# Optimization experiments

Measured on AMD Instinct MI355X. Metric: run time of the kernel, lower is better.

The kernel has to match this reference:

```python
import jax, jax.numpy as jnp
import numpy as np

DIM = 2048
N_HEADS = 16
HEAD_DIM = DIM // N_HEADS
# torch.nn.RMSNorm(eps=None) uses torch.finfo(fp32).eps
RMS_EPS = 1.1920928955078125e-07


def rmsnorm(x, weight):
    # x: [..., Hd]; normalize over last dim, learned scale
    var = jnp.mean(jnp.square(x), axis=-1, keepdims=True)
    return x * jax.lax.rsqrt(var + RMS_EPS) * weight


def setup_inputs() -> dict:
    key = jax.random.key(0)
    ks = jax.random.split(key, 10)
    B, T, D = 4, 2048, DIM
    s = 1.0 / np.sqrt(D)
    return {
        "x": jax.random.normal(ks[0], (B, T, D), dtype=jnp.float32),
        "Wq": jax.random.normal(ks[1], (D, D), dtype=jnp.float32) * s,
        "bq": jnp.zeros((D,), dtype=jnp.float32),
        "Wk": jax.random.normal(ks[2], (D, D), dtype=jnp.float32) * s,
        "bk": jnp.zeros((D,), dtype=jnp.float32),
        "Wv": jax.random.normal(ks[3], (D, D), dtype=jnp.float32) * s,
        "bv": jnp.zeros((D,), dtype=jnp.float32),
        "q_norm_w": jnp.ones((HEAD_DIM,), dtype=jnp.float32),
        "k_norm_w": jnp.ones((HEAD_DIM,), dtype=jnp.float32),
        "Wo": jax.random.normal(ks[4], (D, D), dtype=jnp.float32) * s,
        "bo": jnp.zeros((D,), dtype=jnp.float32),
    }


def reference(x, Wq, bq, Wk, bk, Wv, bv, q_norm_w, k_norm_w, Wo, bo):
    B, T, D = x.shape
    H, Hd = N_HEADS, HEAD_DIM
    # Q/K/V projections (torch Linear: x @ W.T + b)
    q = (x @ Wq.T + bq).reshape(B, T, H, Hd)
    k = (x @ Wk.T + bk).reshape(B, T, H, Hd)
    v = (x @ Wv.T + bv).reshape(B, T, H, Hd)
    # per-head RMSNorm on Q and K
    q = rmsnorm(q, q_norm_w)
    k = rmsnorm(k, k_norm_w)
    # full (non-causal) attention per batch element; scale = 1/sqrt(Hd)
    scale = 1.0 / np.sqrt(Hd)
    scores = jnp.einsum("bqhd,bkhd->bhqk", q, k) * scale
    probs = jax.nn.softmax(scores, axis=-1)
    out = jnp.einsum("bhqk,bkhd->bqhd", probs, v).reshape(B, T, D)
    return out @ Wo.T + bo
```

## Files before the change

### kernel.cpp

```cpp
#include <hip/hip_runtime.h>
#include <cstddef>
#include <cstdint>


typedef __attribute__((ext_vector_type(8))) short sh8;
typedef __attribute__((ext_vector_type(4))) float fx4;
typedef __attribute__((ext_vector_type(4))) unsigned short us4;
typedef __attribute__((ext_vector_type(4))) float f4;
typedef __attribute__((ext_vector_type(2))) unsigned uix2;
typedef unsigned short u16;

#define DEVI __device__ __forceinline__

DEVI u16 f2bf(float f) {
  union { float f; unsigned u; } v; v.f = f;
  return (u16)((v.u + 0x7FFFu + ((v.u >> 16) & 1u)) >> 16);
}
DEVI float bf2f(u16 h) {
  union { unsigned u; float f; } v; v.u = ((unsigned)h) << 16;
  return v.f;
}
DEVI void gload16(const void* g, void* l) {
  __builtin_amdgcn_global_load_lds((const __attribute__((address_space(1))) void*)g,
                                   (__attribute__((address_space(3))) void*)l, 16, 0, 0);
}

__global__ __launch_bounds__(256) void k_cvt(const float* __restrict__ in,
                                             u16* __restrict__ out, int n4) {
  int i = blockIdx.x * 256 + threadIdx.x;
  if (i >= n4) return;
  f4 v = ((const f4*)in)[i];
  us4 o;
  o[0] = f2bf(v[0]); o[1] = f2bf(v[1]); o[2] = f2bf(v[2]); o[3] = f2bf(v[3]);
  ((us4*)out)[i] = o;
}

__global__ __launch_bounds__(256) void k_cvt_w(const float* __restrict__ w0, const float* __restrict__ w1,
                                               const float* __restrict__ w2, const float* __restrict__ w3,
                                               u16* __restrict__ o0, u16* __restrict__ o1,
                                               u16* __restrict__ o2, u16* __restrict__ o3) {
  const int which = blockIdx.y;
  const float* in = which == 0 ? w0 : which == 1 ? w1 : which == 2 ? w2 : w3;
  u16* out = which == 0 ? o0 : which == 1 ? o1 : which == 2 ? o2 : o3;
  int i = blockIdx.x * 256 + threadIdx.x;
  f4 v = ((const f4*)in)[i];
  us4 o;
  o[0] = f2bf(v[0]); o[1] = f2bf(v[1]); o[2] = f2bf(v[2]); o[3] = f2bf(v[3]);
  ((us4*)out)[i] = o;
}

DEVI void stRA(const u16* __restrict__ Ag, int m0, u16* L, int q, int kt, int tid) {
  const int rl = tid >> 3, cc = tid & 7;
#pragma unroll
  for (int j = 0; j < 2; ++j) {
    const int row = j * 128 + q * 64 + rl;
    const int g = cc ^ (row & 7);
    gload16(Ag + (size_t)(m0 + row) * 2048 + kt * 64 + g * 8,
            (char*)L + ((size_t)row * 8 + cc) * 16);
  }
}
DEVI void stRB(const u16* __restrict__ Bg, int n0, u16* L, int q, int kt, int tid) {
  const int rl = tid >> 3, cc = tid & 7;
#pragma unroll
  for (int j = 0; j < 2; ++j) {
    const int row = (j * 2 + (rl >> 5)) * 64 + q * 32 + (rl & 31);
    const int g = cc ^ (row & 7);
    gload16(Bg + (size_t)(n0 + row) * 2048 + kt * 64 + g * 8,
            (char*)L + ((size_t)row * 8 + cc) * 16);
  }
}

DEVI void rdA4(sh8 (&af)[4][2], const u16* L, int mi0, int ln, int hi) {
#pragma unroll
  for (int m = 0; m < 4; ++m)
#pragma unroll
    for (int kk = 0; kk < 2; ++kk)
      af[m][kk] = *(const sh8*)&L[(size_t)((mi0 + m) * 16 + ln) * 64 +
                                  (((kk * 4 + hi) ^ (ln & 7)) * 8)];
}
DEVI void rdB2(sh8 (&bf)[2][2], const u16* L, int row0, int ln, int hi) {
#pragma unroll
  for (int n = 0; n < 2; ++n)
#pragma unroll
    for (int kk = 0; kk < 2; ++kk)
      bf[n][kk] = *(const sh8*)&L[(size_t)(row0 + n * 16 + ln) * 64 +
                                  (((kk * 4 + hi) ^ (ln & 7)) * 8)];
}

#define MFMA_BF16 __builtin_amdgcn_mfma_f32_16x16x32_bf16
#define MMQ(MB, NB, AF, BF)                                                  \
  _Pragma("unroll") for (int kk = 0; kk < 2; ++kk)                           \
  _Pragma("unroll") for (int m2 = 0; m2 < 4; ++m2)                           \
  _Pragma("unroll") for (int n2 = 0; n2 < 2; ++n2)                           \
    acc[MB + m2][NB + n2] =                                                  \
        MFMA_BF16(AF[m2][kk], BF[n2][kk], acc[MB + m2][NB + n2], 0, 0, 0);

#define PH_OPEN()                                              \
  __builtin_amdgcn_s_barrier();                                \
  asm volatile("s_waitcnt lgkmcnt(0)" ::: "memory");           \
  __builtin_amdgcn_sched_barrier(0);                           \
  __builtin_amdgcn_s_setprio(1)
#define PH_CLOSE()                                             \
  __builtin_amdgcn_s_setprio(0);                               \
  __builtin_amdgcn_s_barrier()

DEVI void g256_loop(const u16* __restrict__ Ag, const u16* __restrict__ Bg,
                    int m0, int n0,
                    u16 (&LA)[2][16384], u16 (&LB)[2][16384],
                    fx4 (&acc)[8][4]) {
  constexpr int NI = 16;
  const int tid = threadIdx.x;
  const int lane = tid & 63, ln = lane & 15, hi = lane >> 4;
  const int wid = tid >> 6, wr = wid >> 2, wc = wid & 3;
  const int hB = wc >> 1, rBb = (wc & 1) * 64;
  const u16* A0 = &LA[0][(size_t)wr * 128 * 64];
  const u16* A1 = &LA[1][(size_t)wr * 128 * 64];
  const int rB0 = hB * 128 + rBb;

  stRA(Ag, m0, &LA[0][0], 0, 0, tid);
  stRB(Bg, n0, &LB[0][0], 0, 0, tid);
  stRA(Ag, m0, &LA[0][0], 1, 0, tid);
  stRB(Bg, n0, &LB[0][0], 1, 0, tid);
  stRA(Ag, m0, &LA[1][0], 0, 1, tid);
  stRB(Bg, n0, &LB[1][0], 0, 1, tid);
  asm volatile("s_waitcnt vmcnt(4)" ::: "memory");
  __builtin_amdgcn_s_barrier();

  sh8 af[4][2], bflo[2][2], bfhi[2][2];

  for (int i = 0; i < NI; ++i) {
    const int ta = 2 * i, tb = 2 * i + 1;
    const bool stg = (i + 1 < NI);

    rdA4(af, A0, 0, ln, hi);
    rdB2(bflo, &LB[0][0], rB0, ln, hi);
    stRA(Ag, m0, &LA[1][0], 1, tb, tid);
    PH_OPEN(); MMQ(0, 0, af, bflo); PH_CLOSE();

    rdB2(bfhi, &LB[0][0], rB0 + 32, ln, hi);
    stRB(Bg, n0, &LB[1][0], 1, tb, tid);
    PH_OPEN(); MMQ(0, 2, af, bfhi); PH_CLOSE();

    rdA4(af, A0, 4, ln, hi);
    if (stg) stRA(Ag, m0, &LA[0][0], 0, ta + 2, tid);
    PH_OPEN(); MMQ(4, 0, af, bflo); PH_CLOSE();

    if (stg) stRB(Bg, n0, &LB[0][0], 0, ta + 2, tid);
    PH_OPEN(); MMQ(4, 2, af, bfhi);
    __builtin_amdgcn_s_setprio(0);
    if (i + 1 < NI) asm volatile("s_waitcnt vmcnt(4)" ::: "memory");
    else            asm volatile("s_waitcnt vmcnt(0)" ::: "memory");
    __builtin_amdgcn_s_barrier();

    rdA4(af, A1, 0, ln, hi);
    rdB2(bflo, &LB[1][0], rB0, ln, hi);
    if (stg) stRB(Bg, n0, &LB[0][0], 1, ta + 2, tid);
    PH_OPEN(); MMQ(0, 0, af, bflo); PH_CLOSE();

    rdB2(bfhi, &LB[1][0], rB0 + 32, ln, hi);
    if (stg) stRA(Ag, m0, &LA[0][0], 1, ta + 2, tid);
    PH_OPEN(); MMQ(0, 2, af, bfhi); PH_CLOSE();

    rdA4(af, A1, 4, ln, hi);
    if (stg) stRA(Ag, m0, &LA[1][0], 0, tb + 2, tid);
    PH_OPEN(); MMQ(4, 0, af, bflo); PH_CLOSE();

    if (stg) stRB(Bg, n0, &LB[1][0], 0, tb + 2, tid);
    PH_OPEN(); MMQ(4, 2, af, bfhi);
    __builtin_amdgcn_s_setprio(0);
    asm volatile("s_waitcnt vmcnt(4)" ::: "memory");
    __builtin_amdgcn_s_barrier();
  }
}

__global__ __launch_bounds__(512, 2) void k_gemm_qkv(
    const u16* __restrict__ A,
    const u16* __restrict__ W0, const u16* __restrict__ W1, const u16* __restrict__ W2,
    const float* __restrict__ b0, const float* __restrict__ b1, const float* __restrict__ b2,
    u16* __restrict__ O0, u16* __restrict__ O1, u16* __restrict__ O2) {
  __shared__ __align__(16) u16 LA[2][16384];
  __shared__ __align__(16) u16 LB[2][16384];
  int f = blockIdx.x + (blockIdx.y << 3) + (blockIdx.z << 8);
  f = (f & 7) * 96 + (f >> 3);
  const int z = f >> 8, rem = f & 255;
  const int m0 = (rem >> 3) * 256, n0 = (rem & 7) * 256;
  const u16* Bw = z == 0 ? W0 : z == 1 ? W1 : W2;
  const float* bias = z == 0 ? b0 : z == 1 ? b1 : b2;
  u16* Cout = z == 0 ? O0 : z == 1 ? O1 : O2;

  fx4 acc[8][4] = {};
  g256_loop(A, Bw, m0, n0, LA, LB, acc);

  const int tid = threadIdx.x;
  const int lane = tid & 63, ln = lane & 15, hi = lane >> 4;
  const int wid = tid >> 6, wr = wid >> 2, wc = wid & 3;
#pragma unroll
  for (int mi = 0; mi < 8; ++mi) {
#pragma unroll
    for (int nj = 0; nj < 4; ++nj) {
      const int col = n0 + wc * 64 + nj * 16 + ln;
      const float bv = bias[col];
      const int h = col >> 7, d = col & 127;
#pragma unroll
      for (int j = 0; j < 4; ++j) {
        const int row = m0 + wr * 128 + mi * 16 + hi * 4 + j;
        const int b = row >> 11, trow = row & 2047;
        Cout[((((size_t)b * 16 + h) * 2048) + trow) * 128 + d] = f2bf(acc[mi][nj][j] + bv);
      }
    }
  }
}

__global__ __launch_bounds__(512, 2) void k_gemm_out(const u16* __restrict__ A,
                                                     const u16* __restrict__ Bw,
                                                     const float* __restrict__ bias,
                                                     float* __restrict__ C) {
  __shared__ __align__(16) u16 LA[2][16384];
  __shared__ __align__(16) u16 LB[2][16384];
  int f = blockIdx.x + (blockIdx.y << 3);
  f = (f & 7) * 32 + (f >> 3);
  const int m0 = (f >> 3) * 256, n0 = (f & 7) * 256;

  fx4 acc[8][4] = {};
  g256_loop(A, Bw, m0, n0, LA, LB, acc);

  const int tid = threadIdx.x;
  const int lane = tid & 63, ln = lane & 15, hi = lane >> 4;
  const int wid = tid >> 6, wr = wid >> 2, wc = wid & 3;
#pragma unroll
  for (int mi = 0; mi < 8; ++mi) {
#pragma unroll
    for (int nj = 0; nj < 4; ++nj) {
      const int col = n0 + wc * 64 + nj * 16 + ln;
      const float bv = bias[col];
#pragma unroll
      for (int j = 0; j < 4; ++j) {
        const int row = m0 + wr * 128 + mi * 16 + hi * 4 + j;
        C[(size_t)row * 2048 + col] = acc[mi][nj][j] + bv;
      }
    }
  }
}

__global__ __launch_bounds__(256) void k_rms2(u16* __restrict__ Qb,
                                              u16* __restrict__ Kb,
                                              const float* __restrict__ qw,
                                              const float* __restrict__ kw) {
  const int which = blockIdx.y;
  u16* X = which ? Kb : Qb;
  const float* w = which ? kw : qw;
  const float scale = which ? 1.0f : 0.12751745047f;
  const int row = blockIdx.x * 4 + (threadIdx.x >> 6);
  const int lane = threadIdx.x & 63;
  unsigned* p = (unsigned*)(X + (size_t)row * 128) + lane;
  const unsigned u = *p;
  float a = bf2f((u16)(u & 0xffffu));
  float b = bf2f((u16)(u >> 16));
  float ss = a * a + b * b;
#pragma unroll
  for (int m = 1; m < 64; m <<= 1) ss += __shfl_xor(ss, m);
  const float r = rsqrtf(ss * (1.0f / 128.0f) + 1.1920928955078125e-07f) * scale;
  const float w0 = w[lane * 2], w1 = w[lane * 2 + 1];
  *p = (unsigned)f2bf(a * r * w0) | ((unsigned)f2bf(b * r * w1) << 16);
}

__global__ __launch_bounds__(256) void k_transpose(const u16* __restrict__ V,
                                                   u16* __restrict__ Vt) {
  __shared__ u16 tile[64][65];
  const int bh = blockIdx.z;
  const int d0 = blockIdx.y * 64, t0 = blockIdx.x * 64;
  const int cg = threadIdx.x & 15, rr = threadIdx.x >> 4;
  const u16* Vb = V + ((size_t)bh * 2048 + t0) * 128 + d0;
#pragma unroll
  for (int i = 0; i < 4; ++i) {
    const int r = rr + i * 16;
    us4 v = *(const us4*)(Vb + (size_t)r * 128 + cg * 4);
    tile[r][cg * 4 + 0] = v[0];
    tile[r][cg * 4 + 1] = v[1];
    tile[r][cg * 4 + 2] = v[2];
    tile[r][cg * 4 + 3] = v[3];
  }
  __syncthreads();
  u16* Ob = Vt + ((size_t)bh * 128 + d0) * 2048 + t0;
#pragma unroll
  for (int i = 0; i < 4; ++i) {
    const int d = rr + i * 16;
    us4 v;
    v[0] = tile[cg * 4 + 0][d];
    v[1] = tile[cg * 4 + 1][d];
    v[2] = tile[cg * 4 + 2][d];
    v[3] = tile[cg * 4 + 3][d];
    *(us4*)(Ob + (size_t)d * 2048 + cg * 4) = v;
  }
}

__global__ __launch_bounds__(256, 2) void k_attn(const u16* __restrict__ Q,
                                                 const u16* __restrict__ Kt,
                                                 const u16* __restrict__ Vt,
                                                 u16* __restrict__ Aout) {
  constexpr int T = 2048, Hd = 128;
  __shared__ __align__(16) u16 Ks[2][64 * 128];
  __shared__ __align__(16) u16 Vs[2][128 * 64];
  __shared__ __align__(16) u16 Ps[4 * 32 * 64];
  const int tid = threadIdx.x;
  const int w = tid >> 6, lane = tid & 63;
  const int ln = lane & 15, hi = lane >> 4;
  const int bh = blockIdx.y;
  const int q0 = blockIdx.x * 128 + w * 32;

  const u16* Kgb = Kt + (size_t)bh * T * Hd;
  const u16* Vgb = Vt + (size_t)bh * Hd * T;
  u16* Pw = Ps + w * 2048;

  sh8 qf[2][4];
  const u16* Qb = Q + ((size_t)bh * T + q0) * Hd;
#pragma unroll
  for (int mi = 0; mi < 2; ++mi)
#pragma unroll
    for (int ks = 0; ks < 4; ++ks)
      qf[mi][ks] = *(const sh8*)(Qb + (size_t)(mi * 16 + ln) * Hd + ks * 32 + hi * 8);

  fx4 o[2][8] = {};
  float lsum[2] = {0.0f, 0.0f};

  auto stage = [&](int buf, int t0) {
#pragma unroll
    for (int i = 0; i < 4; ++i) {
      const int c = i * 256 + tid;
      const int r = c >> 4, cc = (c & 15) ^ (r & 7);
      gload16(Kgb + (size_t)(t0 + r) * Hd + cc * 8, (char*)&Ks[buf][0] + c * 16);
    }
#pragma unroll
    for (int i = 0; i < 4; ++i) {
      const int c = i * 256 + tid;
      const int r = c >> 3, cc = (c & 7) ^ (r & 7);
      gload16(Vgb + (size_t)r * T + t0 + cc * 8, (char*)&Vs[buf][0] + c * 16);
    }
  };

  stage(0, 0);
  __syncthreads();
  int cur = 0;

  for (int t0 = 0; t0 < T; t0 += 64) {
    if (t0 + 64 < T) stage(cur ^ 1, t0 + 64);

#pragma unroll
    for (int ni = 0; ni < 4; ++ni) {
      sh8 kf[4];
#pragma unroll
      for (int ks = 0; ks < 4; ++ks)
        kf[ks] = *(const sh8*)&Ks[cur][(((ni * 16 + ln) * 128) + ks * 32 + hi * 8) ^ ((ln & 7) << 3)];
      fx4 st[2] = {};
#pragma unroll
      for (int mi = 0; mi < 2; ++mi)
#pragma unroll
        for (int ks = 0; ks < 4; ++ks)
          st[mi] = MFMA_BF16(kf[ks], qf[mi][ks], st[mi], 0, 0, 0);
#pragma unroll
      for (int mi = 0; mi < 2; ++mi) {
        const float p0 = __builtin_amdgcn_exp2f(st[mi][0] - 17.31234049066756f);
        const float p1 = __builtin_amdgcn_exp2f(st[mi][1] - 17.31234049066756f);
        const float p2 = __builtin_amdgcn_exp2f(st[mi][2] - 17.31234049066756f);
        const float p3 = __builtin_amdgcn_exp2f(st[mi][3] - 17.31234049066756f);
        lsum[mi] += (p0 + p1) + (p2 + p3);
        const unsigned lo = (unsigned)f2bf(p0) | ((unsigned)f2bf(p1) << 16);
        const unsigned hw = (unsigned)f2bf(p2) | ((unsigned)f2bf(p3) << 16);
        const int idx = (((mi * 16 + ln) * 64) + ni * 16 + hi * 4) ^ ((ln & 7) << 3);
        *(uix2*)&Pw[idx] = (uix2){lo, hw};
      }
    }

#pragma unroll
    for (int ks = 0; ks < 2; ++ks) {
      sh8 pf[2];
#pragma unroll
      for (int mi = 0; mi < 2; ++mi)
        pf[mi] = *(const sh8*)&Pw[(((mi * 16 + ln) * 64) + ks * 32 + hi * 8) ^ ((ln & 7) << 3)];
#pragma unroll
      for (int di = 0; di < 8; ++di) {
        const sh8 vf = *(const sh8*)&Vs[cur][(((di * 16 + ln) * 64) + ks * 32 + hi * 8) ^ ((ln & 7) << 3)];
#pragma unroll
        for (int mi = 0; mi < 2; ++mi)
          o[mi][di] = MFMA_BF16(pf[mi], vf, o[mi][di], 0, 0, 0);
      }
    }

    __syncthreads();
    cur ^= 1;
  }

#pragma unroll
  for (int mi = 0; mi < 2; ++mi) {
    lsum[mi] += __shfl_xor(lsum[mi], 16);
    lsum[mi] += __shfl_xor(lsum[mi], 32);
  }

  const int b = bh >> 4, h = bh & 15;
  u16* Ob = Aout + ((size_t)b * T + q0) * 2048 + h * 128;
#pragma unroll
  for (int mi = 0; mi < 2; ++mi) {
    fx4 rv;
#pragma unroll
    for (int j = 0; j < 4; ++j)
      rv[j] = 1.0f / __shfl(lsum[mi], 20 * (lane >> 4) + j);
#pragma unroll
    for (int di = 0; di < 8; ++di) {
      fx4 val = o[mi][di] * rv;
#pragma unroll
      for (int j = 0; j < 4; ++j)
        Ob[(size_t)(mi * 16 + hi * 4 + j) * 2048 + di * 16 + ln] = f2bf(val[j]);
    }
  }
}

extern "C" void kernel_launch(void* const* d_in, const int* in_sizes, int n_in,
                              void* d_out, int out_size, void* d_ws, size_t ws_size,
                              hipStream_t stream) {
  const float* x   = (const float*)d_in[0];
  const float* Wq  = (const float*)d_in[1];
  const float* bq  = (const float*)d_in[2];
  const float* Wk  = (const float*)d_in[3];
  const float* bk  = (const float*)d_in[4];
  const float* Wv  = (const float*)d_in[5];
  const float* bv  = (const float*)d_in[6];
  const float* qnw = (const float*)d_in[7];
  const float* knw = (const float*)d_in[8];
  const float* Wo  = (const float*)d_in[9];
  const float* bo  = (const float*)d_in[10];
  float* out = (float*)d_out;

  const size_t SZ_X = 33554432;
  const size_t SZ_W = 8388608;
  char* ws = (char*)d_ws;
  u16* xb  = (u16*)(ws);
  u16* Wqb = (u16*)(ws + SZ_X);
  u16* Wkb = (u16*)(ws + SZ_X + SZ_W);
  u16* Wvb = (u16*)(ws + SZ_X + 2 * SZ_W);
  u16* Wob = (u16*)(ws + SZ_X + 3 * SZ_W);
  u16* Qb  = (u16*)(ws + SZ_X + 4 * SZ_W);
  u16* Kb  = (u16*)(ws + 2 * SZ_X + 4 * SZ_W);
  u16* Vb  = (u16*)(ws + 3 * SZ_X + 4 * SZ_W);
  u16* Vtb = (u16*)(ws + 4 * SZ_X + 4 * SZ_W);
  u16* AOb = Vb;

  k_cvt<<<16384, 256, 0, stream>>>(x, xb, 4194304);
  k_cvt_w<<<dim3(4096, 4), 256, 0, stream>>>(Wq, Wk, Wv, Wo, Wqb, Wkb, Wvb, Wob);
  k_gemm_qkv<<<dim3(8, 32, 3), 512, 0, stream>>>(xb, Wqb, Wkb, Wvb, bq, bk, bv, Qb, Kb, Vb);
  k_rms2<<<dim3(32768, 2), 256, 0, stream>>>(Qb, Kb, qnw, knw);
  k_transpose<<<dim3(32, 2, 64), 256, 0, stream>>>(Vb, Vtb);
  k_attn<<<dim3(16, 64), 256, 0, stream>>>(Qb, Kb, Vtb, AOb);
  k_gemm_out<<<dim3(8, 32), 512, 0, stream>>>(AOb, Wob, bo, out);
}
```

Baseline: 494.1 us.

## Fuse per-head RMSNorm and V transpose into QKV GEMM epilogue

Moves the per-head RMSNorm of Q and K into the QKV GEMM epilogue. Each head's 128 columns span two wave columns, so the sum of squares is reduced across lanes and exchanged through LDS. The V output is now written directly in transposed [b,h,d,t] layout with 4-element vector stores. Two separate kernels and their extra global read/write passes go away, at the cost of a heavier epilogue and two extra block barriers.

After: 457.5 us. 7.4% less time.

```diff
diff --git a/kernel.cpp b/kernel.cpp
--- a/kernel.cpp
+++ b/kernel.cpp
@@ -177,6 +177,7 @@
     const u16* __restrict__ A,
     const u16* __restrict__ W0, const u16* __restrict__ W1, const u16* __restrict__ W2,
     const float* __restrict__ b0, const float* __restrict__ b1, const float* __restrict__ b2,
+    const float* __restrict__ qn, const float* __restrict__ kn,
     u16* __restrict__ O0, u16* __restrict__ O1, u16* __restrict__ O2) {
   __shared__ __align__(16) u16 LA[2][16384];
   __shared__ __align__(16) u16 LB[2][16384];
@@ -194,18 +195,78 @@
   const int tid = threadIdx.x;
   const int lane = tid & 63, ln = lane & 15, hi = lane >> 4;
   const int wid = tid >> 6, wr = wid >> 2, wc = wid & 3;
-#pragma unroll
-  for (int mi = 0; mi < 8; ++mi) {
-#pragma unroll
-    for (int nj = 0; nj < 4; ++nj) {
-      const int col = n0 + wc * 64 + nj * 16 + ln;
-      const float bv = bias[col];
-      const int h = col >> 7, d = col & 127;
+
+#pragma unroll
+  for (int nj = 0; nj < 4; ++nj) {
+    const float bv = bias[n0 + wc * 64 + nj * 16 + ln];
+#pragma unroll
+    for (int mi = 0; mi < 8; ++mi)
+#pragma unroll
+      for (int j = 0; j < 4; ++j) acc[mi][nj][j] += bv;
+  }
+
+  if (z < 2) {
+    float ss[8][4];
+#pragma unroll
+    for (int mi = 0; mi < 8; ++mi)
 #pragma unroll
       for (int j = 0; j < 4; ++j) {
-        const int row = m0 + wr * 128 + mi * 16 + hi * 4 + j;
-        const int b = row >> 11, trow = row & 2047;
-        Cout[((((size_t)b * 16 + h) * 2048) + trow) * 128 + d] = f2bf(acc[mi][nj][j] + bv);
+        float s = 0.0f;
+#pragma unroll
+        for (int nj = 0; nj < 4; ++nj) s += acc[mi][nj][j] * acc[mi][nj][j];
+#pragma unroll
+        for (int m = 1; m < 16; m <<= 1) s += __shfl_xor(s, m);
+        ss[mi][j] = s;
+      }
+    float* sums = (float*)&LA[0][0];
+    __syncthreads();
+    if (ln == 0) {
+#pragma unroll
+      for (int mi = 0; mi < 8; ++mi)
+#pragma unroll
+        for (int j = 0; j < 4; ++j)
+          sums[(wr * 4 + wc) * 128 + mi * 16 + hi * 4 + j] = ss[mi][j];
+    }
+    __syncthreads();
+    const float zscale = z == 0 ? 0.12751745047f : 1.0f;
+    const float* wnorm = z == 0 ? qn : kn;
+#pragma unroll
+    for (int mi = 0; mi < 8; ++mi)
+#pragma unroll
+      for (int j = 0; j < 4; ++j) {
+        const float tot = ss[mi][j] +
+            sums[(wr * 4 + (wc ^ 1)) * 128 + mi * 16 + hi * 4 + j];
+        ss[mi][j] = rsqrtf(tot * (1.0f / 128.0f) + 1.1920928955078125e-07f) * zscale;
+      }
+#pragma unroll
+    for (int mi = 0; mi < 8; ++mi) {
+#pragma unroll
+      for (int nj = 0; nj < 4; ++nj) {
+        const int col = n0 + wc * 64 + nj * 16 + ln;
+        const int h = col >> 7, d = col & 127;
+        const float wv = wnorm[d];
+#pragma unroll
+        for (int j = 0; j < 4; ++j) {
+          const int row = m0 + wr * 128 + mi * 16 + hi * 4 + j;
+          const int b = row >> 11, t = row & 2047;
+          Cout[((((size_t)b * 16 + h) * 2048) + t) * 128 + d] =
+              f2bf(acc[mi][nj][j] * ss[mi][j] * wv);
+        }
+      }
+    }
+  } else {
+#pragma unroll
+    for (int mi = 0; mi < 8; ++mi) {
+#pragma unroll
+      for (int nj = 0; nj < 4; ++nj) {
+        const int col = n0 + wc * 64 + nj * 16 + ln;
+        const int h = col >> 7, d = col & 127;
+        const int row0 = m0 + wr * 128 + mi * 16 + hi * 4;
+        const int b = row0 >> 11, t = row0 & 2047;
+        us4 v;
+#pragma unroll
+        for (int j = 0; j < 4; ++j) v[j] = f2bf(acc[mi][nj][j]);
+        *(us4*)&Cout[((((size_t)b * 16 + h) * 128) + d) * 2048 + t] = v;
       }
     }
   }
@@ -239,58 +300,6 @@
         C[(size_t)row * 2048 + col] = acc[mi][nj][j] + bv;
       }
     }
-  }
-}
-
-__global__ __launch_bounds__(256) void k_rms2(u16* __restrict__ Qb,
-                                              u16* __restrict__ Kb,
-                                              const float* __restrict__ qw,
-                                              const float* __restrict__ kw) {
-  const int which = blockIdx.y;
-  u16* X = which ? Kb : Qb;
-  const float* w = which ? kw : qw;
-  const float scale = which ? 1.0f : 0.12751745047f;
-  const int row = blockIdx.x * 4 + (threadIdx.x >> 6);
-  const int lane = threadIdx.x & 63;
-  unsigned* p = (unsigned*)(X + (size_t)row * 128) + lane;
-  const unsigned u = *p;
-  float a = bf2f((u16)(u & 0xffffu));
-  float b = bf2f((u16)(u >> 16));
-  float ss = a * a + b * b;
-#pragma unroll
-  for (int m = 1; m < 64; m <<= 1) ss += __shfl_xor(ss, m);
-  const float r = rsqrtf(ss * (1.0f / 128.0f) + 1.1920928955078125e-07f) * scale;
-  const float w0 = w[lane * 2], w1 = w[lane * 2 + 1];
-  *p = (unsigned)f2bf(a * r * w0) | ((unsigned)f2bf(b * r * w1) << 16);
-}
-
-__global__ __launch_bounds__(256) void k_transpose(const u16* __restrict__ V,
-                                                   u16* __restrict__ Vt) {
-  __shared__ u16 tile[64][65];
-  const int bh = blockIdx.z;
-  const int d0 = blockIdx.y * 64, t0 = blockIdx.x * 64;
-  const int cg = threadIdx.x & 15, rr = threadIdx.x >> 4;
-  const u16* Vb = V + ((size_t)bh * 2048 + t0) * 128 + d0;
-#pragma unroll
-  for (int i = 0; i < 4; ++i) {
-    const int r = rr + i * 16;
-    us4 v = *(const us4*)(Vb + (size_t)r * 128 + cg * 4);
-    tile[r][cg * 4 + 0] = v[0];
-    tile[r][cg * 4 + 1] = v[1];
-    tile[r][cg * 4 + 2] = v[2];
-    tile[r][cg * 4 + 3] = v[3];
-  }
-  __syncthreads();
-  u16* Ob = Vt + ((size_t)bh * 128 + d0) * 2048 + t0;
-#pragma unroll
-  for (int i = 0; i < 4; ++i) {
-    const int d = rr + i * 16;
-    us4 v;
-    v[0] = tile[cg * 4 + 0][d];
-    v[1] = tile[cg * 4 + 1][d];
-    v[2] = tile[cg * 4 + 2][d];
-    v[3] = tile[cg * 4 + 3][d];
-    *(us4*)(Ob + (size_t)d * 2048 + cg * 4) = v;
   }
 }
 
@@ -446,9 +455,8 @@
 
   k_cvt<<<16384, 256, 0, stream>>>(x, xb, 4194304);
   k_cvt_w<<<dim3(4096, 4), 256, 0, stream>>>(Wq, Wk, Wv, Wo, Wqb, Wkb, Wvb, Wob);
-  k_gemm_qkv<<<dim3(8, 32, 3), 512, 0, stream>>>(xb, Wqb, Wkb, Wvb, bq, bk, bv, Qb, Kb, Vb);
-  k_rms2<<<dim3(32768, 2), 256, 0, stream>>>(Qb, Kb, qnw, knw);
-  k_transpose<<<dim3(32, 2, 64), 256, 0, stream>>>(Vb, Vtb);
+  k_gemm_qkv<<<dim3(8, 32, 3), 512, 0, stream>>>(xb, Wqb, Wkb, Wvb, bq, bk, bv,
+                                                 qnw, knw, Qb, Kb, Vtb);
   k_attn<<<dim3(16, 64), 256, 0, stream>>>(Qb, Kb, Vtb, AOb);
   k_gemm_out<<<dim3(8, 32), 512, 0, stream>>>(AOb, Wob, bo, out);
 }
```
